# Kernel optimization log

Measured on AMD Instinct MI355X. Metric: run time of the kernel, lower is better.

The kernel has to match this reference:

```python
import jax, jax.numpy as jnp
import numpy as np

H = 1024
M = 4096
K = 64            # max_memory_updates_per_step
THRESH = 0.5      # surprise_threshold
EPS = 1e-12


def setup_inputs() -> dict:
    key = jax.random.key(0)
    ks = jax.random.split(key, 5)
    B, S = 4, 2048
    return {
        "hidden_states": jax.random.normal(ks[0], (B, S, H), dtype=jnp.float32),
        "ln_gamma": jnp.ones((H,), jnp.float32),
        "ln_beta": jnp.zeros((H,), jnp.float32),
        "Wq": jax.random.normal(ks[1], (H, H), jnp.float32) * 0.02,
        "bq": jnp.zeros((H,), jnp.float32),
        "Wo": jax.random.normal(ks[2], (H, H), jnp.float32) * 0.02,
        "bo": jnp.zeros((H,), jnp.float32),
        "memory": jax.random.normal(ks[3], (M, H), jnp.float32),
        "importance_scores": jax.random.uniform(ks[4], (M,), jnp.float32),
    }


def _layer_norm(x, g, b):
    mu = jnp.mean(x, axis=-1, keepdims=True)
    var = jnp.mean(jnp.square(x - mu), axis=-1, keepdims=True)
    return (x - mu) * jax.lax.rsqrt(var + EPS) * g + b


def reference(hidden_states, ln_gamma, ln_beta, Wq, bq, Wo, bo, memory, importance_scores):
    # LayerNorm
    norm = _layer_norm(hidden_states, ln_gamma, ln_beta)  # [B,S,H]

    # Surprise measure (detached): mean |x| over hidden dim
    surprise = jnp.mean(jnp.abs(jax.lax.stop_gradient(norm)), axis=-1)  # [B,S]

    # --- surprise-based memory update (buffers; no gradient, training mode) ---
    flat_h = jax.lax.stop_gradient(norm).reshape(-1, H)   # [B*S, H]
    flat_s = surprise.reshape(-1)                          # [B*S]
    # top-K surprises, descending (matches where>thr -> sort desc -> take K)
    top_vals, top_idx = jax.lax.top_k(flat_s, K)
    valid = top_vals > THRESH                              # entries below threshold: no write
    # K slots with smallest importance, ascending importance order
    _, slots = jax.lax.top_k(-importance_scores, K)
    new_rows = flat_h[top_idx]                             # [K, H]
    old_rows = memory[slots]                               # [K, H]
    mem = memory.at[slots].set(jnp.where(valid[:, None], new_rows, old_rows))  # [M,H]

    # --- query memory ---
    q = jnp.einsum("bsh,oh->bso", norm, Wq) + bq           # query_proj
    sim = jnp.einsum("bsh,mh->bsm", q, mem)                # [B,S,M]
    attn = jax.nn.softmax(sim, axis=-1)
    retrieved = jnp.einsum("bsm,mh->bsh", attn, mem)       # [B,S,H]
    mem_out = jnp.einsum("bsh,oh->bso", retrieved, Wo) + bo  # output_proj

    # dropout in eval mode = identity; residual add
    return hidden_states + mem_out
```

## Files before the change

kernel.cpp:

```cpp
#include <hip/hip_runtime.h>

#define H 1024
#define MMEM 4096
#define NTOK 8192
#define KTOP 64
#define FTHRESH 0.5f

typedef _Float16 half8 __attribute__((ext_vector_type(8)));
typedef float vf4 __attribute__((ext_vector_type(4)));

__device__ __forceinline__ short f2h(float x){
  union { _Float16 h; short s; } u; u.h = (_Float16)x; return u.s;
}
__device__ __forceinline__ float h2f(short s){
  union { _Float16 h; short s; } u; u.s = s; return (float)u.h;
}
__device__ __forceinline__ unsigned fkey_of(float x){
  unsigned u = __float_as_uint(x);
  return (u & 0x80000000u) ? ~u : (u | 0x80000000u);
}
__device__ __forceinline__ float val_of(unsigned k){
  unsigned u = (k & 0x80000000u) ? (k & 0x7fffffffu) : ~k;
  return __uint_as_float(u);
}

__device__ __forceinline__ void gload_lds16(const short* g, short* l){
  __builtin_amdgcn_global_load_lds(
      (const __attribute__((address_space(1))) unsigned int*)g,
      (__attribute__((address_space(3))) unsigned int*)l, 16, 0, 0);
}

__global__ __launch_bounds__(256) void ln_kernel(
    const float* __restrict__ hs, const float* __restrict__ g, const float* __restrict__ be,
    short* __restrict__ n16, float* __restrict__ surprise)
{
  int row = blockIdx.x, tid = threadIdx.x;
  long base = (long)row * H;
  float4 x = ((const float4*)(hs + base))[tid];
  float s1 = x.x + x.y + x.z + x.w;
  float s2 = x.x*x.x + x.y*x.y + x.z*x.z + x.w*x.w;
  __shared__ float r1[4], r2[4], r3[4];
  int w = tid >> 6, lane = tid & 63;
  for (int o = 32; o; o >>= 1){ s1 += __shfl_down(s1, o); s2 += __shfl_down(s2, o); }
  if (lane == 0){ r1[w] = s1; r2[w] = s2; }
  __syncthreads();
  float S1 = r1[0]+r1[1]+r1[2]+r1[3];
  float S2 = r2[0]+r2[1]+r2[2]+r2[3];
  float mean = S1 * (1.0f/H);
  float var  = S2 * (1.0f/H) - mean*mean;
  float rinv = rsqrtf(var + 1e-12f);
  float4 gg = ((const float4*)g)[tid];
  float4 bb = ((const float4*)be)[tid];
  float4 n;
  n.x = (x.x-mean)*rinv*gg.x + bb.x;
  n.y = (x.y-mean)*rinv*gg.y + bb.y;
  n.z = (x.z-mean)*rinv*gg.z + bb.z;
  n.w = (x.w-mean)*rinv*gg.w + bb.w;
  float sa = fabsf(n.x)+fabsf(n.y)+fabsf(n.z)+fabsf(n.w);
  for (int o = 32; o; o >>= 1) sa += __shfl_down(sa, o);
  if (lane == 0) r3[w] = sa;
  __syncthreads();
  if (tid == 0) surprise[row] = (r3[0]+r3[1]+r3[2]+r3[3]) * (1.0f/H);
  short4 h4;
  h4.x = f2h(n.x); h4.y = f2h(n.y); h4.z = f2h(n.z); h4.w = f2h(n.w);
  ((short4*)(n16 + base))[tid] = h4;
}

__global__ __launch_bounds__(256) void topk_local(
    const float* __restrict__ surprise, const float* __restrict__ imp,
    unsigned long long* __restrict__ cand_s, unsigned long long* __restrict__ cand_i)
{
  __shared__ unsigned long long s[256];
  int b = blockIdx.x, tid = threadIdx.x;
  int maxmode = (b < 32);
  int gidx = maxmode ? (b*256 + tid) : ((b-32)*256 + tid);
  float x = maxmode ? surprise[gidx] : imp[gidx];
  unsigned k = fkey_of(x);
  if (!maxmode) k = ~k;
  s[tid] = ((unsigned long long)k << 32) | (unsigned)(8191 - gidx);
  __syncthreads();
  for (int kk = 2; kk <= 256; kk <<= 1)
    for (int j = kk >> 1; j > 0; j >>= 1){
      int i = tid, ixj = i ^ j;
      if (ixj > i){
        bool asc = ((i & kk) == 0);
        unsigned long long a = s[i], c = s[ixj];
        if ((a < c) == asc){ s[i] = c; s[ixj] = a; }
      }
      __syncthreads();
    }
  if (tid < 64){
    if (maxmode) cand_s[b*64 + tid] = s[tid];
    else         cand_i[(b-32)*64 + tid] = s[tid];
  }
}

__global__ __launch_bounds__(256) void topk_merge(
    const unsigned long long* __restrict__ cand_s, const unsigned long long* __restrict__ cand_i,
    float* __restrict__ top_vals, int* __restrict__ top_idx, int* __restrict__ slots)
{
  __shared__ unsigned long long s[2048];
  int tid = threadIdx.x;
  int N = (blockIdx.x == 0) ? 2048 : 1024;
  const unsigned long long* src = (blockIdx.x == 0) ? cand_s : cand_i;
  for (int i = tid; i < N; i += 256) s[i] = src[i];
  __syncthreads();
  for (int kk = 2; kk <= N; kk <<= 1)
    for (int j = kk >> 1; j > 0; j >>= 1){
      for (int i = tid; i < N; i += 256){
        int ixj = i ^ j;
        if (ixj > i){
          bool asc = ((i & kk) == 0);
          unsigned long long a = s[i], c = s[ixj];
          if ((a < c) == asc){ s[i] = c; s[ixj] = a; }
        }
      }
      __syncthreads();
    }
  if (tid < 64){
    unsigned long long p = s[tid];
    int gi = 8191 - (int)(p & 0xffffffffu);
    if (blockIdx.x == 0){
      top_vals[tid] = val_of((unsigned)(p >> 32));
      top_idx[tid] = gi;
    } else {
      slots[tid] = gi;
    }
  }
}

__global__ __launch_bounds__(256) void prep_all_kernel(
    const float* __restrict__ mem, const float* __restrict__ Wq, const float* __restrict__ Wo,
    short* __restrict__ m16, short* __restrict__ memT,
    short* __restrict__ wq_h, short* __restrict__ wq_l, short* __restrict__ wo16)
{
  __shared__ __align__(16) short t[64][66];
  int b = blockIdx.x, tid = threadIdx.x;
  if (b < 1024){
    int r0 = (b >> 4) * 64, c0 = (b & 15) * 64;
    #pragma unroll
    for (int k = 0; k < 4; ++k){
      int idx = k*256 + tid;
      int r = idx >> 4, c4 = (idx & 15) * 4;
      float4 x = *(const float4*)&mem[(long)(r0+r)*H + c0 + c4];
      short4 h;
      h.x = f2h(x.x); h.y = f2h(x.y); h.z = f2h(x.z); h.w = f2h(x.w);
      *(short4*)&m16[(long)(r0+r)*H + c0 + c4] = h;
      t[r][c4] = h.x; t[r][c4+1] = h.y; t[r][c4+2] = h.z; t[r][c4+3] = h.w;
    }
    __syncthreads();
    #pragma unroll
    for (int k = 0; k < 4; ++k){
      int idx = k*256 + tid;
      int c = idx >> 4, r4 = (idx & 15) * 4;
      short4 h;
      h.x = t[r4][c]; h.y = t[r4+1][c]; h.z = t[r4+2][c]; h.w = t[r4+3][c];
      *(short4*)&memT[(long)(c0+c)*MMEM + r0 + r4] = h;
    }
  } else if (b < 2048){
    long i = (long)(b - 1024) * 256 + tid;
    float4 x = ((const float4*)Wq)[i];
    short4 h, l;
    h.x = f2h(x.x); l.x = f2h(x.x - h2f(h.x));
    h.y = f2h(x.y); l.y = f2h(x.y - h2f(h.y));
    h.z = f2h(x.z); l.z = f2h(x.z - h2f(h.z));
    h.w = f2h(x.w); l.w = f2h(x.w - h2f(h.w));
    ((short4*)wq_h)[i] = h;
    ((short4*)wq_l)[i] = l;
  } else {
    long i = (long)(b - 2048) * 256 + tid;
    float4 x = ((const float4*)Wo)[i];
    short4 h;
    h.x = f2h(x.x); h.y = f2h(x.y); h.z = f2h(x.z); h.w = f2h(x.w);
    ((short4*)wo16)[i] = h;
  }
}

__global__ __launch_bounds__(256) void update_kernel(
    const float* __restrict__ top_vals, const int* __restrict__ top_idx, const int* __restrict__ slots,
    const float* __restrict__ hs, const float* __restrict__ g, const float* __restrict__ be,
    short* __restrict__ m16, short* __restrict__ memT)
{
  int i = blockIdx.x;
  if (top_vals[i] <= FTHRESH) return;
  int s = slots[i], r = top_idx[i];
  int tid = threadIdx.x, w = tid >> 6, lane = tid & 63;
  long base = (long)r * H;
  float4 x = ((const float4*)(hs + base))[tid];
  float s1 = x.x + x.y + x.z + x.w;
  float s2 = x.x*x.x + x.y*x.y + x.z*x.z + x.w*x.w;
  __shared__ float r1[4], r2[4];
  for (int o = 32; o; o >>= 1){ s1 += __shfl_down(s1, o); s2 += __shfl_down(s2, o); }
  if (lane == 0){ r1[w] = s1; r2[w] = s2; }
  __syncthreads();
  float S1 = r1[0]+r1[1]+r1[2]+r1[3];
  float S2 = r2[0]+r2[1]+r2[2]+r2[3];
  float mean = S1 * (1.0f/H);
  float var  = S2 * (1.0f/H) - mean*mean;
  float rinv = rsqrtf(var + 1e-12f);
  float4 gg = ((const float4*)g)[tid];
  float4 bb = ((const float4*)be)[tid];
  short4 h4;
  h4.x = f2h((x.x-mean)*rinv*gg.x + bb.x);
  h4.y = f2h((x.y-mean)*rinv*gg.y + bb.y);
  h4.z = f2h((x.z-mean)*rinv*gg.z + bb.z);
  h4.w = f2h((x.w-mean)*rinv*gg.w + bb.w);
  ((short4*)(m16 + (long)s*H))[tid] = h4;
  long c4 = (long)tid * 4;
  memT[(c4+0)*MMEM + s] = h4.x;
  memT[(c4+1)*MMEM + s] = h4.y;
  memT[(c4+2)*MMEM + s] = h4.z;
  memT[(c4+3)*MMEM + s] = h4.w;
}

__global__ __launch_bounds__(256) void bias_kernel(
    const float* __restrict__ bq, const short* __restrict__ m16, float* __restrict__ biasM)
{
  int tid = threadIdx.x, w = tid >> 6, lane = tid & 63;
  int m = blockIdx.x*4 + w;
  const short* ph = m16 + (long)m*H;
  float s = 0.f;
  for (int j = 0; j < 16; ++j){
    int h = lane + j*64;
    s += bq[h] * h2f(ph[h]);
  }
  for (int o = 32; o; o >>= 1) s += __shfl_down(s, o);
  if (lane == 0) biasM[m] = s;
}

template<int SPLIT, int MODE>
__global__ __launch_bounds__(256) void gemm128(
    const short* __restrict__ A,
    const short* __restrict__ Bh, const short* __restrict__ Bl,
    int K, int N,
    short* __restrict__ O1,
    float* __restrict__ Of, const float* __restrict__ resid, const float* __restrict__ biasN)
{
  __shared__ short sA[128*64];
  __shared__ short sBh[128*64];
  __shared__ short sBl[SPLIT ? 128*64 : 64];
  int tid = threadIdx.x, w = tid >> 6, lane = tid & 63, ln = lane & 15, quad = lane >> 4;
  int wr = w >> 1, wc = w & 1;
  int nwgx = gridDim.x;
  int nwg  = nwgx * gridDim.y;
  int lin  = blockIdx.y * nwgx + blockIdx.x;
  int nl   = (lin & 7) * (nwg >> 3) + (lin >> 3);
  long m0 = (long)(nl / nwgx) * 128, n0 = (long)(nl % nwgx) * 128;
  long Kl = K;
  vf4 acc[4][4];
  #pragma unroll
  for (int i = 0; i < 4; ++i) for (int j = 0; j < 4; ++j) for (int r = 0; r < 4; ++r) acc[i][j][r] = 0.0f;

  for (long kk = 0; kk < Kl; kk += 64){
    #pragma unroll
    for (int j = 0; j < 4; ++j){
      int f = (w*4 + j)*64 + lane;
      int row = f >> 3, c8 = f & 7;
      long go = kk + (long)((c8 ^ (row & 7)) * 8);
      gload_lds16(A  + (m0+row)*Kl + go, sA  + (w*4+j)*512);
      gload_lds16(Bh + (n0+row)*Kl + go, sBh + (w*4+j)*512);
      if (SPLIT) gload_lds16(Bl + (n0+row)*Kl + go, sBl + (w*4+j)*512);
    }
    __syncthreads();
    #pragma unroll
    for (int ks = 0; ks < 64; ks += 32){
      int cbase = (ks >> 3) + quad;
      half8 bh[4], bl[4];
      #pragma unroll
      for (int j = 0; j < 4; ++j){
        int rb = wc*64 + j*16 + ln;
        int cb = cbase ^ (rb & 7);
        bh[j] = *(const half8*)&sBh[rb*64 + cb*8];
        if (SPLIT) bl[j] = *(const half8*)&sBl[rb*64 + cb*8];
      }
      #pragma unroll
      for (int i = 0; i < 4; ++i){
        int ra = wr*64 + i*16 + ln;
        int ca = cbase ^ (ra & 7);
        half8 a = *(const half8*)&sA[ra*64 + ca*8];
        #pragma unroll
        for (int j = 0; j < 4; ++j){
          acc[i][j] = __builtin_amdgcn_mfma_f32_16x16x32_f16(a, bh[j], acc[i][j], 0, 0, 0);
          if (SPLIT)
            acc[i][j] = __builtin_amdgcn_mfma_f32_16x16x32_f16(a, bl[j], acc[i][j], 0, 0, 0);
        }
      }
    }
    __syncthreads();
  }

  #pragma unroll
  for (int i = 0; i < 4; ++i){
    #pragma unroll
    for (int j = 0; j < 4; ++j){
      #pragma unroll
      for (int r = 0; r < 4; ++r){
        long row = m0 + wr*64 + i*16 + quad*4 + r;
        long col = n0 + wc*64 + j*16 + ln;
        float v = acc[i][j][r];
        if (MODE == 1){
          O1[row*(long)N + col] = f2h(v + biasN[col]);
        } else if (MODE == 2){
          O1[row*(long)N + col] = f2h(v);
        } else {
          Of[row*(long)N + col] = v + resid[row*(long)N + col] + biasN[col];
        }
      }
    }
  }
}

__global__ __launch_bounds__(256) void softmax_kernel(short* __restrict__ simP)
{
  long row = blockIdx.x;
  int tid = threadIdx.x, w = tid >> 6, lane = tid & 63;
  half8* ptr = (half8*)(simP + row*MMEM);
  float xf[16];
  float mx = -1e30f;
  #pragma unroll
  for (int j = 0; j < 2; ++j){
    half8 x = ptr[tid + j*256];
    #pragma unroll
    for (int e = 0; e < 8; ++e){ float f = (float)x[e]; xf[j*8+e] = f; mx = fmaxf(mx, f); }
  }
  for (int o = 32; o; o >>= 1) mx = fmaxf(mx, __shfl_xor(mx, o));
  __shared__ float rmax[4], rsum[4];
  if (lane == 0) rmax[w] = mx;
  __syncthreads();
  mx = fmaxf(fmaxf(rmax[0], rmax[1]), fmaxf(rmax[2], rmax[3]));
  float p[16], s = 0.f;
  #pragma unroll
  for (int k = 0; k < 16; ++k){ p[k] = __expf(xf[k] - mx); s += p[k]; }
  for (int o = 32; o; o >>= 1) s += __shfl_xor(s, o);
  if (lane == 0) rsum[w] = s;
  __syncthreads();
  float inv = 1.0f / (rsum[0]+rsum[1]+rsum[2]+rsum[3]);
  #pragma unroll
  for (int j = 0; j < 2; ++j){
    half8 o8;
    #pragma unroll
    for (int e = 0; e < 8; ++e) o8[e] = (_Float16)(p[j*8+e] * inv);
    ptr[tid + j*256] = o8;
  }
}

extern "C" void kernel_launch(void* const* d_in, const int* in_sizes, int n_in,
                              void* d_out, int out_size, void* d_ws, size_t ws_size,
                              hipStream_t stream)
{
  const float* hs  = (const float*)d_in[0];
  const float* gam = (const float*)d_in[1];
  const float* bet = (const float*)d_in[2];
  const float* Wq  = (const float*)d_in[3];
  const float* bq  = (const float*)d_in[4];
  const float* Wo  = (const float*)d_in[5];
  const float* bo  = (const float*)d_in[6];
  const float* mem = (const float*)d_in[7];
  const float* imp = (const float*)d_in[8];
  float* out = (float*)d_out;

  char* ws = (char*)d_ws;
  short* n16   = (short*)(ws);
  short* q16   = (short*)(ws + (16ull<<20));
  short* m16   = (short*)(ws + (32ull<<20));
  short* memT  = (short*)(ws + (40ull<<20));
  short* simP  = (short*)(ws + (48ull<<20));
  short* vwoT  = (short*)(ws + (112ull<<20));
  short* wq_h  = (short*)(ws + (128ull<<20));
  short* wq_l  = (short*)(ws + (130ull<<20));
  short* wo16  = (short*)(ws + (132ull<<20));
  char*  tail  = ws + (134ull<<20);
  float* biasM    = (float*)tail;
  float* surprise = (float*)(tail + (64<<10));
  float* top_vals = (float*)(tail + (128<<10));
  int*   top_idx  = (int*)  (tail + (129<<10));
  int*   slots    = (int*)  (tail + (130<<10));
  unsigned long long* cand_s = (unsigned long long*)(tail + (132<<10));
  unsigned long long* cand_i = (unsigned long long*)(tail + (148<<10));

  ln_kernel<<<NTOK, 256, 0, stream>>>(hs, gam, bet, n16, surprise);
  topk_local<<<48, 256, 0, stream>>>(surprise, imp, cand_s, cand_i);
  topk_merge<<<2, 256, 0, stream>>>(cand_s, cand_i, top_vals, top_idx, slots);
  prep_all_kernel<<<3072, 256, 0, stream>>>(mem, Wq, Wo, m16, memT, wq_h, wq_l, wo16);
  update_kernel<<<KTOP, 256, 0, stream>>>(top_vals, top_idx, slots, hs, gam, bet, m16, memT);
  bias_kernel<<<1024, 256, 0, stream>>>(bq, m16, biasM);
  gemm128<0,2><<<dim3(32,8), 256, 0, stream>>>(
      wo16, m16, m16, H, MMEM, vwoT, nullptr, nullptr, nullptr);
  gemm128<2,2><<<dim3(8,64), 256, 0, stream>>>(
      n16, wq_h, wq_l, H, H, q16, nullptr, nullptr, nullptr);
  gemm128<0,1><<<dim3(32,64), 256, 0, stream>>>(
      q16, m16, m16, H, MMEM, simP, nullptr, nullptr, biasM);
  softmax_kernel<<<NTOK, 256, 0, stream>>>(simP);
  gemm128<0,3><<<dim3(8,64), 256, 0, stream>>>(
      simP, vwoT, vwoT, MMEM, H, nullptr, out, hs, bo);
}
```

Measured before the change: 428.3 us.

## Add 256x256-tile pipelined GEMM for the query-memory similarity product

Adds a new 512-thread GEMM kernel with 256x256 output tiles, double-buffered 128KB LDS, staged async global-to-LDS loads interleaved with MFMA phases, and XCD-aware block remapping. It replaces the 128x128 GEMM for the largest matmul (q times memory, 8192x4096x1024). The aim is more operand reuse per LDS load and better overlap of loads with compute. The cost is heavy register and LDS pressure that limits occupancy, and the prefetch indices wrap around at the end of the K loop.

```diff
diff --git a/kernel.cpp b/kernel.cpp
--- a/kernel.cpp
+++ b/kernel.cpp
@@ -310,6 +310,133 @@
   }
 }
 
+template<int MODE>
+__global__ __launch_bounds__(512, 2) void gemm256(
+    const short* __restrict__ A, const short* __restrict__ B,
+    int K, int N,
+    short* __restrict__ O1, float* __restrict__ Of,
+    const float* __restrict__ resid, const float* __restrict__ biasN)
+{
+  extern __shared__ short lds[];
+  int tid = threadIdx.x, w = tid >> 6, lane = tid & 63, ln = lane & 15, quad = lane >> 4;
+  int wr = w >> 2, wc = w & 3;
+  int nwgx = gridDim.x, nwg = nwgx * gridDim.y;
+  int lin = blockIdx.y * nwgx + blockIdx.x;
+  int nl  = (lin & 7) * (nwg >> 3) + (lin >> 3);
+  long m0 = (long)(nl / nwgx) * 256, n0 = (long)(nl % nwgx) * 256;
+  long Kl = K;
+  int NT = K >> 6;
+
+  auto STAGE = [&](const short* __restrict__ G, long rowbase, long kt, short* ldsbase){
+    #pragma unroll
+    for (int i = 0; i < 2; ++i){
+      int f = i*512 + tid;
+      int row = f >> 3, c8 = f & 7;
+      long go = kt + (long)((c8 ^ (row & 7)) * 8);
+      gload_lds16(G + (rowbase + row)*Kl + go, ldsbase + i*4096 + w*512);
+    }
+  };
+
+  vf4 acc[4][4][2];
+  #pragma unroll
+  for (int p = 0; p < 4; ++p)
+    for (int i = 0; i < 4; ++i)
+      for (int j = 0; j < 2; ++j)
+        for (int r = 0; r < 4; ++r) acc[p][i][j][r] = 0.0f;
+
+  {
+    int t1 = (NT > 1) ? 1 : 0;
+    STAGE(A, m0 + 0,   0, lds + 0);
+    STAGE(B, n0 + 0,   0, lds + 16384);
+    STAGE(B, n0 + 128, 0, lds + 16384 + 8192);
+    STAGE(A, m0 + 128, 0, lds + 8192);
+    STAGE(A, m0 + 0,   (long)t1*64, lds + 32768);
+    STAGE(B, n0 + 0,   (long)t1*64, lds + 32768 + 16384);
+  }
+  asm volatile("s_waitcnt vmcnt(8)" ::: "memory");
+  asm volatile("s_barrier" ::: "memory");
+
+  for (int t = 0; t < NT; ++t){
+    int cur = t & 1;
+    short* bA = lds + cur*32768;
+    short* bB = bA + 16384;
+    short* oA = lds + (cur^1)*32768;
+    short* oB = oA + 16384;
+    int t1 = t + 1; if (t1 >= NT) t1 -= NT;
+    int t2 = t + 2; if (t2 >= NT) t2 -= NT;
+    long kt1 = (long)t1 * 64, kt2 = (long)t2 * 64;
+    #pragma unroll
+    for (int p = 0; p < 4; ++p){
+      const short* sAh = bA + (p >> 1)*8192;
+      const short* sBh = bB + (p & 1)*8192;
+      half8 af[4][2], bf[2][2];
+      #pragma unroll
+      for (int ks = 0; ks < 2; ++ks){
+        int cbase = ks*4 + quad;
+        #pragma unroll
+        for (int j = 0; j < 2; ++j){
+          int rb = wc*32 + j*16 + ln;
+          bf[j][ks] = *(const half8*)&sBh[rb*64 + (cbase ^ (rb & 7))*8];
+        }
+        #pragma unroll
+        for (int i = 0; i < 4; ++i){
+          int ra = wr*64 + i*16 + ln;
+          af[i][ks] = *(const half8*)&sAh[ra*64 + (cbase ^ (ra & 7))*8];
+        }
+      }
+      if (p == 0)      STAGE(B, n0 + 128, kt1, oB + 8192);
+      else if (p == 1) STAGE(A, m0 + 128, kt1, oA + 8192);
+      else if (p == 2) STAGE(A, m0 + 0,   kt2, bA + 0);
+      else             STAGE(B, n0 + 0,   kt2, bB + 0);
+      asm volatile("s_barrier" ::: "memory");
+      asm volatile("s_waitcnt lgkmcnt(0)" ::: "memory");
+      __builtin_amdgcn_sched_barrier(0);
+      __builtin_amdgcn_s_setprio(1);
+      #pragma unroll
+      for (int i = 0; i < 4; ++i){
+        #pragma unroll
+        for (int j = 0; j < 2; ++j){
+          acc[p][i][j] = __builtin_amdgcn_mfma_f32_16x16x32_f16(af[i][0], bf[j][0], acc[p][i][j], 0, 0, 0);
+          acc[p][i][j] = __builtin_amdgcn_mfma_f32_16x16x32_f16(af[i][1], bf[j][1], acc[p][i][j], 0, 0, 0);
+        }
+      }
+      __builtin_amdgcn_s_setprio(0);
+      asm volatile("s_waitcnt vmcnt(8)" ::: "memory");
+      asm volatile("s_barrier" ::: "memory");
+    }
+  }
+
+  float bn[2][2];
+  if (MODE != 2){
+    #pragma unroll
+    for (int bh = 0; bh < 2; ++bh)
+      for (int j = 0; j < 2; ++j)
+        bn[bh][j] = biasN[n0 + bh*128 + wc*32 + j*16 + ln];
+  }
+  #pragma unroll
+  for (int p = 0; p < 4; ++p){
+    #pragma unroll
+    for (int i = 0; i < 4; ++i){
+      #pragma unroll
+      for (int j = 0; j < 2; ++j){
+        #pragma unroll
+        for (int r = 0; r < 4; ++r){
+          long row = m0 + (p >> 1)*128 + wr*64 + i*16 + quad*4 + r;
+          long col = n0 + (p & 1)*128 + wc*32 + j*16 + ln;
+          float v = acc[p][i][j][r];
+          if (MODE == 1){
+            O1[row*(long)N + col] = f2h(v + bn[p & 1][j]);
+          } else if (MODE == 2){
+            O1[row*(long)N + col] = f2h(v);
+          } else {
+            Of[row*(long)N + col] = v + resid[row*(long)N + col] + bn[p & 1][j];
+          }
+        }
+      }
+    }
+  }
+}
+
 __global__ __launch_bounds__(256) void softmax_kernel(short* __restrict__ simP)
 {
   long row = blockIdx.x;
@@ -378,6 +505,13 @@
   unsigned long long* cand_s = (unsigned long long*)(tail + (132<<10));
   unsigned long long* cand_i = (unsigned long long*)(tail + (148<<10));
 
+  static bool attr_done = false;
+  if (!attr_done){
+    hipFuncSetAttribute(reinterpret_cast<const void*>(&gemm256<1>),
+                        hipFuncAttributeMaxDynamicSharedMemorySize, 131072);
+    attr_done = true;
+  }
+
   ln_kernel<<<NTOK, 256, 0, stream>>>(hs, gam, bet, n16, surprise);
   topk_local<<<48, 256, 0, stream>>>(surprise, imp, cand_s, cand_i);
   topk_merge<<<2, 256, 0, stream>>>(cand_s, cand_i, top_vals, top_idx, slots);
@@ -388,8 +522,8 @@
       wo16, m16, m16, H, MMEM, vwoT, nullptr, nullptr, nullptr);
   gemm128<2,2><<<dim3(8,64), 256, 0, stream>>>(
       n16, wq_h, wq_l, H, H, q16, nullptr, nullptr, nullptr);
-  gemm128<0,1><<<dim3(32,64), 256, 0, stream>>>(
-      q16, m16, m16, H, MMEM, simP, nullptr, nullptr, biasM);
+  gemm256<1><<<dim3(16,32), 512, 131072, stream>>>(
+      q16, m16, H, MMEM, simP, nullptr, nullptr, biasM);
   softmax_kernel<<<NTOK, 256, 0, stream>>>(simP);
   gemm128<0,3><<<dim3(8,64), 256, 0, stream>>>(
       simP, vwoT, vwoT, MMEM, H, nullptr, out, hs, bo);
```

New measurement: 429.8 us. Within noise of the previous version (+0.4%).
